# Performance work log

Hardware: AMD Instinct MI355X
Metric: run time of the kernel (lower is better)

The kernel has to match this reference:

```python
import jax, jax.numpy as jnp
import numpy as np

V = 50000  # word vocab (table has V+1 rows)
L = 256    # number of labels
B = 128    # batch
T = 512    # sequence length


def setup_inputs() -> dict:
    key = jax.random.key(0)
    k1, k2, k3 = jax.random.split(key, 3)
    emis = jax.random.normal(k1, (V + 1, L), dtype=jnp.float32)
    trans = jax.random.normal(k2, (L, L), dtype=jnp.float32)
    words = jax.random.randint(k3, (B, T), 0, V, dtype=jnp.int32)
    return {"emis": emis, "trans": trans, "words": words}


def reference(emis, trans, words):
    # Gather all emission scores up front: [B, T, L]
    e = emis[words]
    alpha0 = e[:, 0]  # [B, L]

    def step(alpha_prev, e_t):
        # alpha_new[b, c] = logsumexp_p( e_t[b, c] + trans[c, p] + alpha_prev[b, p] )
        scores = e_t[:, :, None] + trans[None, :, :] + alpha_prev[:, None, :]  # [B, L, L]
        return jax.nn.logsumexp(scores, axis=2), None

    # scan over time: e[:, 1:] -> time-major [T-1, B, L]
    alpha_last, _ = jax.lax.scan(step, alpha0, jnp.swapaxes(e[:, 1:], 0, 1))
    log_Z = jax.nn.logsumexp(alpha_last, axis=1).sum()  # scalar, summed over batch
    return log_Z
```

## Files before the change

### kernel.cpp

```cpp
#include <hip/hip_runtime.h>

#define NB 128
#define NT 512
#define NL 256
#define NWG NB

typedef float f32x4 __attribute__((ext_vector_type(4)));
typedef int   i32x8 __attribute__((ext_vector_type(8)));
typedef int   i32x4v __attribute__((ext_vector_type(4)));

#define EASTRIDE 272
#define GEXP 7
#define E8M0_ONE 127
#define INV_LN2 1.4426950408889634f
#define LN2 0.6931471805599453f

__device__ inline float log2_fast(float x) {
#if __has_builtin(__builtin_amdgcn_logf)
    return __builtin_amdgcn_logf(x);
#else
    return __log2f(x);
#endif
}
__device__ inline float exp2_fast(float x) {
#if __has_builtin(__builtin_amdgcn_exp2f)
    return __builtin_amdgcn_exp2f(x);
#else
    return exp2f(x);
#endif
}

__device__ inline void barrier_lds_only() {
    asm volatile("s_waitcnt lgkmcnt(0)" ::: "memory");
    __builtin_amdgcn_s_barrier();
    asm volatile("" ::: "memory");
}

__device__ inline unsigned pk_fp8x4(float a, float b, float c, float d) {
    int w = __builtin_amdgcn_cvt_pk_fp8_f32(a, b, 0, false);
    w     = __builtin_amdgcn_cvt_pk_fp8_f32(c, d, w, true);
    return (unsigned)w;
}

__device__ inline i32x8 ld_b256(const unsigned char* p) {
    i32x4v lo = *reinterpret_cast<const i32x4v*>(p);
    i32x4v hi = *reinterpret_cast<const i32x4v*>(p + 16);
    i32x8 r;
    r[0] = lo[0]; r[1] = lo[1]; r[2] = lo[2]; r[3] = lo[3];
    r[4] = hi[0]; r[5] = hi[1]; r[6] = hi[2]; r[7] = hi[3];
    return r;
}

__global__ __launch_bounds__(512, 2) void crf_forward(
    const float* __restrict__ emis,
    const float* __restrict__ trans,
    const int*   __restrict__ words,
    float*       __restrict__ bout)
{
    const int tid = threadIdx.x;
    const int l   = tid & 63;
    const int wv  = tid >> 6;
    const int g   = l >> 4;
    const int b   = l & 15;

    __shared__ __align__(16) unsigned char ea[2][EASTRIDE];
    __shared__ __align__(16) float pm[2][8];
    __shared__ int wlds[NT];

    const int wrow = blockIdx.x * NT;

    wlds[tid] = words[wrow + tid];

    i32x8 afr[2][2];
    #pragma unroll
    for (int T = 0; T < 2; ++T) {
        const int row = wv * 32 + T * 16 + b;
        #pragma unroll
        for (int kt = 0; kt < 2; ++kt) {
            const float* src = trans + row * NL + kt * 128 + g * 32;
            i32x8 a;
            #pragma unroll
            for (int w = 0; w < 8; ++w) {
                float4 v = *reinterpret_cast<const float4*>(src + w * 4);
                a[w] = (int)pk_fp8x4(__expf(v.x), __expf(v.y),
                                     __expf(v.z), __expf(v.w));
            }
            afr[T][kt] = a;
        }
    }

    const int w0 = words[wrow + 0];
    const int w1 = words[wrow + 1];
    const int w2 = words[wrow + 2];
    const int w3 = words[wrow + 3];
    const int w4 = words[wrow + 4];
    int wregA = words[wrow + 5];
    int wregB = words[wrow + 6];
    int wregC = words[wrow + 7];
    int wregD = words[wrow + 8];

    float S = 0.f;

    {
        const float* e0 = emis + (size_t)w0 * NL + wv * 32 + g * 4;
        float pmax = 0.f;
        unsigned pk[2];
        #pragma unroll
        for (int T = 0; T < 2; ++T) {
            f32x4 v = *reinterpret_cast<const f32x4*>(e0 + T * 16);
            float p0 = exp2_fast(v[0] * INV_LN2);
            float p1 = exp2_fast(v[1] * INV_LN2);
            float p2 = exp2_fast(v[2] * INV_LN2);
            float p3 = exp2_fast(v[3] * INV_LN2);
            pmax = fmaxf(pmax, fmaxf(fmaxf(p0, p1), fmaxf(p2, p3)));
            pk[T] = pk_fp8x4(p0, p1, p2, p3);
        }
        pmax = fmaxf(pmax, __shfl_xor(pmax, 16));
        pmax = fmaxf(pmax, __shfl_xor(pmax, 32));
        if (l == 0) pm[0][wv] = pmax;
        if (b == 0) {
            *reinterpret_cast<unsigned*>(&ea[0][wv * 32 + g * 4])      = pk[0];
            *reinterpret_cast<unsigned*>(&ea[0][wv * 32 + 16 + g * 4]) = pk[1];
        }
    }
    f32x4 pfA[2], pfB[2], pfC[2], pfD[2];
    {
        const float* p;
        p = emis + (size_t)w1 * NL + wv * 32 + g * 4;
        pfA[0] = *(const f32x4*)p; pfA[1] = *(const f32x4*)(p + 16);
        p = emis + (size_t)w2 * NL + wv * 32 + g * 4;
        pfB[0] = *(const f32x4*)p; pfB[1] = *(const f32x4*)(p + 16);
        p = emis + (size_t)w3 * NL + wv * 32 + g * 4;
        pfC[0] = *(const f32x4*)p; pfC[1] = *(const f32x4*)(p + 16);
        p = emis + (size_t)w4 * NL + wv * 32 + g * 4;
        pfD[0] = *(const f32x4*)p; pfD[1] = *(const f32x4*)(p + 16);
    }
    barrier_lds_only();

#define CRF_STEP(t, RD, WR, PF, WREG)                                           \
    {                                                                           \
                         \
        i32x8 bq0 = ld_b256(&ea[RD][g * 32]);                                   \
        i32x8 bq1 = ld_b256(&ea[RD][128 + g * 32]);                             \
        f32x4 pm0 = *reinterpret_cast<const f32x4*>(&pm[RD][0]);                \
        f32x4 pm1 = *reinterpret_cast<const f32x4*>(&pm[RD][4]);                \
        float gm  = fmaxf(fmaxf(fmaxf(pm0[0], pm0[1]), fmaxf(pm0[2], pm0[3])),  \
                          fmaxf(fmaxf(pm1[0], pm1[1]), fmaxf(pm1[2], pm1[3]))); \
        int   kb  = (int)(__builtin_bit_cast(unsigned, gm) >> 23) - (127 - GEXP);\
        S += (float)kb;                                                         \
        float kbf = (float)kb;                                                  \
        f32x4 eC[2] = { PF[0], PF[1] };                                         \
        if ((t) + 4 < NT) {                                                     \
            const float* ep = emis + (size_t)WREG * NL + wv * 32 + g * 4;       \
            PF[0] = *(const f32x4*)ep;  PF[1] = *(const f32x4*)(ep + 16);       \
        }                                                                       \
        if ((t) + 8 < NT) WREG = wlds[(t) + 8];                                 \
                                             \
        f32x4 ex[2];                                                            \
        _Pragma("unroll")                                                       \
        for (int T = 0; T < 2; ++T) {                                           \
            ex[T][0] = exp2_fast(fmaf(eC[T][0], INV_LN2, -kbf));                \
            ex[T][1] = exp2_fast(fmaf(eC[T][1], INV_LN2, -kbf));                \
            ex[T][2] = exp2_fast(fmaf(eC[T][2], INV_LN2, -kbf));                \
            ex[T][3] = exp2_fast(fmaf(eC[T][3], INV_LN2, -kbf));                \
        }                                                                       \
                      \
        f32x4 sA[2];                                                            \
        _Pragma("unroll")                                                       \
        for (int T = 0; T < 2; ++T) {                                           \
            f32x4 z = {0.f, 0.f, 0.f, 0.f};                                     \
            z = __builtin_amdgcn_mfma_scale_f32_16x16x128_f8f6f4(               \
                    afr[T][0], bq0, z, 0, 0, 0, E8M0_ONE, 0, E8M0_ONE);         \
            z = __builtin_amdgcn_mfma_scale_f32_16x16x128_f8f6f4(               \
                    afr[T][1], bq1, z, 0, 0, 0, E8M0_ONE, 0, E8M0_ONE);         \
            sA[T] = z;                                                          \
        }                                                                       \
        float pmax = 0.f;                                                       \
        unsigned pk[2];                                                         \
        _Pragma("unroll")                                                       \
        for (int T = 0; T < 2; ++T) {                                           \
            f32x4 wv4 = sA[T] * ex[T];                                          \
            pmax = fmaxf(pmax, fmaxf(fmaxf(wv4[0], wv4[1]),                     \
                                     fmaxf(wv4[2], wv4[3])));                   \
            pk[T] = pk_fp8x4(wv4[0], wv4[1], wv4[2], wv4[3]);                   \
        }                                                                       \
        pmax = fmaxf(pmax, __shfl_xor(pmax, 16));                               \
        pmax = fmaxf(pmax, __shfl_xor(pmax, 32));                               \
        if (l == 0) pm[WR][wv] = pmax;                                          \
        if (b == 0) {                                                           \
            *reinterpret_cast<unsigned*>(&ea[WR][wv * 32 + g * 4])      = pk[0];\
            *reinterpret_cast<unsigned*>(&ea[WR][wv * 32 + 16 + g * 4]) = pk[1];\
        }                                                                       \
        barrier_lds_only();                                                     \
    }

    int t = 1;
    for (; t + 3 < NT; t += 4) {
        CRF_STEP(t,     0, 1, pfA, wregA);
        CRF_STEP(t + 1, 1, 0, pfB, wregB);
        CRF_STEP(t + 2, 0, 1, pfC, wregC);
        CRF_STEP(t + 3, 1, 0, pfD, wregD);
    }
    CRF_STEP(509, 0, 1, pfA, wregA);
    CRF_STEP(510, 1, 0, pfB, wregB);
    CRF_STEP(511, 0, 1, pfC, wregC);
#undef CRF_STEP

    if (tid < 64) {
        unsigned u = *reinterpret_cast<const unsigned*>(&ea[1][tid * 4]);
        float s = __builtin_amdgcn_cvt_f32_fp8((int)u, 0)
                + __builtin_amdgcn_cvt_f32_fp8((int)u, 1)
                + __builtin_amdgcn_cvt_f32_fp8((int)u, 2)
                + __builtin_amdgcn_cvt_f32_fp8((int)u, 3);
        #pragma unroll
        for (int off = 32; off; off >>= 1) s += __shfl_xor(s, off);
        if (tid == 0) bout[blockIdx.x] = (S + log2_fast(s)) * LN2;
    }
}

__global__ void crf_reduce(const float* __restrict__ bout, float* __restrict__ out)
{
    const int tid = threadIdx.x;
    float v = bout[tid];
    #pragma unroll
    for (int off = 32; off; off >>= 1) v += __shfl_xor(v, off);
    __shared__ float sred[2];
    if ((tid & 63) == 0) sred[tid >> 6] = v;
    __syncthreads();
    if (tid == 0) out[0] = sred[0] + sred[1];
}

extern "C" void kernel_launch(void* const* d_in, const int* in_sizes, int n_in,
                              void* d_out, int out_size, void* d_ws, size_t ws_size,
                              hipStream_t stream)
{
    const float* emis  = (const float*)d_in[0];
    const float* trans = (const float*)d_in[1];
    const int*   words = (const int*)d_in[2];
    float* out  = (float*)d_out;
    float* bout = (float*)d_ws;

    crf_forward<<<NWG, 512, 0, stream>>>(emis, trans, words, bout);
    crf_reduce<<<1, NB, 0, stream>>>(bout, out);
}
```

Baseline: 293.2 us.

## Shorten emission prefetch depth, drop LDS word staging, interleave MFMA chains

Cuts the emission prefetch pipeline from four steps ahead to two, and reads word indices straight from global memory instead of staging them in LDS. The two independent MFMA accumulation chains are interleaved, the exp2 computations are moved ahead of the prefetch load, and the B-operand LDS loads become single 256-bit vector loads. The aim is to lower register pressure and LDS traffic on the serial recurrence's critical path. The risk is that the shallower prefetch exposes more global-load latency on each time step.

```diff
diff --git a/kernel.cpp b/kernel.cpp
--- a/kernel.cpp
+++ b/kernel.cpp
@@ -7,7 +7,6 @@
 
 typedef float f32x4 __attribute__((ext_vector_type(4)));
 typedef int   i32x8 __attribute__((ext_vector_type(8)));
-typedef int   i32x4v __attribute__((ext_vector_type(4)));
 
 #define EASTRIDE 272
 #define GEXP 7
@@ -40,15 +39,6 @@
     int w = __builtin_amdgcn_cvt_pk_fp8_f32(a, b, 0, false);
     w     = __builtin_amdgcn_cvt_pk_fp8_f32(c, d, w, true);
     return (unsigned)w;
-}
-
-__device__ inline i32x8 ld_b256(const unsigned char* p) {
-    i32x4v lo = *reinterpret_cast<const i32x4v*>(p);
-    i32x4v hi = *reinterpret_cast<const i32x4v*>(p + 16);
-    i32x8 r;
-    r[0] = lo[0]; r[1] = lo[1]; r[2] = lo[2]; r[3] = lo[3];
-    r[4] = hi[0]; r[5] = hi[1]; r[6] = hi[2]; r[7] = hi[3];
-    return r;
 }
 
 __global__ __launch_bounds__(512, 2) void crf_forward(
@@ -65,11 +55,9 @@
 
     __shared__ __align__(16) unsigned char ea[2][EASTRIDE];
     __shared__ __align__(16) float pm[2][8];
-    __shared__ int wlds[NT];
-
-    const int wrow = blockIdx.x * NT;
-
-    wlds[tid] = words[wrow + tid];
+
+    const int* ws = words + (size_t)blockIdx.x * NT;
+    const int eoff = wv * 32 + g * 4;
 
     i32x8 afr[2][2];
     #pragma unroll
@@ -89,121 +77,106 @@
         }
     }
 
-    const int w0 = words[wrow + 0];
-    const int w1 = words[wrow + 1];
-    const int w2 = words[wrow + 2];
-    const int w3 = words[wrow + 3];
-    const int w4 = words[wrow + 4];
-    int wregA = words[wrow + 5];
-    int wregB = words[wrow + 6];
-    int wregC = words[wrow + 7];
-    int wregD = words[wrow + 8];
+    const int w0 = ws[0];
+    const int w1 = ws[1];
+    const int w2 = ws[2];
+    int wA = ws[3];
+    int wB = ws[4];
 
     float S = 0.f;
 
     {
-        const float* e0 = emis + (size_t)w0 * NL + wv * 32 + g * 4;
-        float pmax = 0.f;
-        unsigned pk[2];
-        #pragma unroll
-        for (int T = 0; T < 2; ++T) {
-            f32x4 v = *reinterpret_cast<const f32x4*>(e0 + T * 16);
-            float p0 = exp2_fast(v[0] * INV_LN2);
-            float p1 = exp2_fast(v[1] * INV_LN2);
-            float p2 = exp2_fast(v[2] * INV_LN2);
-            float p3 = exp2_fast(v[3] * INV_LN2);
-            pmax = fmaxf(pmax, fmaxf(fmaxf(p0, p1), fmaxf(p2, p3)));
-            pk[T] = pk_fp8x4(p0, p1, p2, p3);
-        }
+        const float* e0 = emis + (size_t)w0 * NL + eoff;
+        f32x4 v0 = *reinterpret_cast<const f32x4*>(e0);
+        f32x4 v1 = *reinterpret_cast<const f32x4*>(e0 + 16);
+        float p00 = exp2_fast(v0[0] * INV_LN2), p01 = exp2_fast(v0[1] * INV_LN2);
+        float p02 = exp2_fast(v0[2] * INV_LN2), p03 = exp2_fast(v0[3] * INV_LN2);
+        float p10 = exp2_fast(v1[0] * INV_LN2), p11 = exp2_fast(v1[1] * INV_LN2);
+        float p12 = exp2_fast(v1[2] * INV_LN2), p13 = exp2_fast(v1[3] * INV_LN2);
+        float pmax = fmaxf(fmaxf(fmaxf(p00, p01), fmaxf(p02, p03)),
+                           fmaxf(fmaxf(p10, p11), fmaxf(p12, p13)));
         pmax = fmaxf(pmax, __shfl_xor(pmax, 16));
         pmax = fmaxf(pmax, __shfl_xor(pmax, 32));
         if (l == 0) pm[0][wv] = pmax;
         if (b == 0) {
-            *reinterpret_cast<unsigned*>(&ea[0][wv * 32 + g * 4])      = pk[0];
-            *reinterpret_cast<unsigned*>(&ea[0][wv * 32 + 16 + g * 4]) = pk[1];
+            *reinterpret_cast<unsigned*>(&ea[0][wv * 32 + g * 4]) =
+                pk_fp8x4(p00, p01, p02, p03);
+            *reinterpret_cast<unsigned*>(&ea[0][wv * 32 + 16 + g * 4]) =
+                pk_fp8x4(p10, p11, p12, p13);
         }
     }
-    f32x4 pfA[2], pfB[2], pfC[2], pfD[2];
+    f32x4 pfA0, pfA1, pfB0, pfB1;
     {
-        const float* p;
-        p = emis + (size_t)w1 * NL + wv * 32 + g * 4;
-        pfA[0] = *(const f32x4*)p; pfA[1] = *(const f32x4*)(p + 16);
-        p = emis + (size_t)w2 * NL + wv * 32 + g * 4;
-        pfB[0] = *(const f32x4*)p; pfB[1] = *(const f32x4*)(p + 16);
-        p = emis + (size_t)w3 * NL + wv * 32 + g * 4;
-        pfC[0] = *(const f32x4*)p; pfC[1] = *(const f32x4*)(p + 16);
-        p = emis + (size_t)w4 * NL + wv * 32 + g * 4;
-        pfD[0] = *(const f32x4*)p; pfD[1] = *(const f32x4*)(p + 16);
+        const float* p1 = emis + (size_t)w1 * NL + eoff;
+        pfA0 = *reinterpret_cast<const f32x4*>(p1);
+        pfA1 = *reinterpret_cast<const f32x4*>(p1 + 16);
+        const float* p2 = emis + (size_t)w2 * NL + eoff;
+        pfB0 = *reinterpret_cast<const f32x4*>(p2);
+        pfB1 = *reinterpret_cast<const f32x4*>(p2 + 16);
     }
     barrier_lds_only();
 
-#define CRF_STEP(t, RD, WR, PF, WREG)                                           \
+#define CRF_STEP(t, RD, WR, PF0, PF1, WREG)                                     \
     {                                                                           \
                          \
-        i32x8 bq0 = ld_b256(&ea[RD][g * 32]);                                   \
-        i32x8 bq1 = ld_b256(&ea[RD][128 + g * 32]);                             \
+        i32x8 bq0 = *reinterpret_cast<const i32x8*>(&ea[RD][g * 32]);           \
+        i32x8 bq1 = *reinterpret_cast<const i32x8*>(&ea[RD][128 + g * 32]);     \
         f32x4 pm0 = *reinterpret_cast<const f32x4*>(&pm[RD][0]);                \
         f32x4 pm1 = *reinterpret_cast<const f32x4*>(&pm[RD][4]);                \
-        float gm  = fmaxf(fmaxf(fmaxf(pm0[0], pm0[1]), fmaxf(pm0[2], pm0[3])),  \
-                          fmaxf(fmaxf(pm1[0], pm1[1]), fmaxf(pm1[2], pm1[3]))); \
-        int   kb  = (int)(__builtin_bit_cast(unsigned, gm) >> 23) - (127 - GEXP);\
+        float gm = fmaxf(fmaxf(fmaxf(pm0[0], pm0[1]), fmaxf(pm0[2], pm0[3])),   \
+                         fmaxf(fmaxf(pm1[0], pm1[1]), fmaxf(pm1[2], pm1[3])));  \
+        int   kb = (int)(__builtin_bit_cast(unsigned, gm) >> 23) - (127 - GEXP);\
         S += (float)kb;                                                         \
         float kbf = (float)kb;                                                  \
-        f32x4 eC[2] = { PF[0], PF[1] };                                         \
-        if ((t) + 4 < NT) {                                                     \
-            const float* ep = emis + (size_t)WREG * NL + wv * 32 + g * 4;       \
-            PF[0] = *(const f32x4*)ep;  PF[1] = *(const f32x4*)(ep + 16);       \
+             \
+        float exa0 = exp2_fast(fmaf(PF0[0], INV_LN2, -kbf));                    \
+        float exa1 = exp2_fast(fmaf(PF0[1], INV_LN2, -kbf));                    \
+        float exa2 = exp2_fast(fmaf(PF0[2], INV_LN2, -kbf));                    \
+        float exa3 = exp2_fast(fmaf(PF0[3], INV_LN2, -kbf));                    \
+        float exb0 = exp2_fast(fmaf(PF1[0], INV_LN2, -kbf));                    \
+        float exb1 = exp2_fast(fmaf(PF1[1], INV_LN2, -kbf));                    \
+        float exb2 = exp2_fast(fmaf(PF1[2], INV_LN2, -kbf));                    \
+        float exb3 = exp2_fast(fmaf(PF1[3], INV_LN2, -kbf));                    \
+        if ((t) + 2 < NT) {                                                     \
+            const float* ep = emis + (size_t)WREG * NL + eoff;                  \
+            PF0 = *reinterpret_cast<const f32x4*>(ep);                          \
+            PF1 = *reinterpret_cast<const f32x4*>(ep + 16);                     \
         }                                                                       \
-        if ((t) + 8 < NT) WREG = wlds[(t) + 8];                                 \
-                                             \
-        f32x4 ex[2];                                                            \
-        _Pragma("unroll")                                                       \
-        for (int T = 0; T < 2; ++T) {                                           \
-            ex[T][0] = exp2_fast(fmaf(eC[T][0], INV_LN2, -kbf));                \
-            ex[T][1] = exp2_fast(fmaf(eC[T][1], INV_LN2, -kbf));                \
-            ex[T][2] = exp2_fast(fmaf(eC[T][2], INV_LN2, -kbf));                \
-            ex[T][3] = exp2_fast(fmaf(eC[T][3], INV_LN2, -kbf));                \
-        }                                                                       \
-                      \
-        f32x4 sA[2];                                                            \
-        _Pragma("unroll")                                                       \
-        for (int T = 0; T < 2; ++T) {                                           \
-            f32x4 z = {0.f, 0.f, 0.f, 0.f};                                     \
-            z = __builtin_amdgcn_mfma_scale_f32_16x16x128_f8f6f4(               \
-                    afr[T][0], bq0, z, 0, 0, 0, E8M0_ONE, 0, E8M0_ONE);         \
-            z = __builtin_amdgcn_mfma_scale_f32_16x16x128_f8f6f4(               \
-                    afr[T][1], bq1, z, 0, 0, 0, E8M0_ONE, 0, E8M0_ONE);         \
-            sA[T] = z;                                                          \
-        }                                                                       \
-        float pmax = 0.f;                                                       \
-        unsigned pk[2];                                                         \
-        _Pragma("unroll")                                                       \
-        for (int T = 0; T < 2; ++T) {                                           \
-            f32x4 wv4 = sA[T] * ex[T];                                          \
-            pmax = fmaxf(pmax, fmaxf(fmaxf(wv4[0], wv4[1]),                     \
-                                     fmaxf(wv4[2], wv4[3])));                   \
-            pk[T] = pk_fp8x4(wv4[0], wv4[1], wv4[2], wv4[3]);                   \
-        }                                                                       \
+        if ((t) + 4 < NT) WREG = ws[(t) + 4];                                   \
+                         \
+        f32x4 z0 = {0.f, 0.f, 0.f, 0.f};                                        \
+        f32x4 z1 = {0.f, 0.f, 0.f, 0.f};                                        \
+        z0 = __builtin_amdgcn_mfma_scale_f32_16x16x128_f8f6f4(                  \
+                 afr[0][0], bq0, z0, 0, 0, 0, E8M0_ONE, 0, E8M0_ONE);           \
+        z1 = __builtin_amdgcn_mfma_scale_f32_16x16x128_f8f6f4(                  \
+                 afr[1][0], bq0, z1, 0, 0, 0, E8M0_ONE, 0, E8M0_ONE);           \
+        z0 = __builtin_amdgcn_mfma_scale_f32_16x16x128_f8f6f4(                  \
+                 afr[0][1], bq1, z0, 0, 0, 0, E8M0_ONE, 0, E8M0_ONE);           \
+        z1 = __builtin_amdgcn_mfma_scale_f32_16x16x128_f8f6f4(                  \
+                 afr[1][1], bq1, z1, 0, 0, 0, E8M0_ONE, 0, E8M0_ONE);           \
+        float v00 = z0[0] * exa0, v01 = z0[1] * exa1;                           \
+        float v02 = z0[2] * exa2, v03 = z0[3] * exa3;                           \
+        float v10 = z1[0] * exb0, v11 = z1[1] * exb1;                           \
+        float v12 = z1[2] * exb2, v13 = z1[3] * exb3;                           \
+        float pmax = fmaxf(fmaxf(fmaxf(v00, v01), fmaxf(v02, v03)),             \
+                           fmaxf(fmaxf(v10, v11), fmaxf(v12, v13)));            \
         pmax = fmaxf(pmax, __shfl_xor(pmax, 16));                               \
         pmax = fmaxf(pmax, __shfl_xor(pmax, 32));                               \
         if (l == 0) pm[WR][wv] = pmax;                                          \
         if (b == 0) {                                                           \
-            *reinterpret_cast<unsigned*>(&ea[WR][wv * 32 + g * 4])      = pk[0];\
-            *reinterpret_cast<unsigned*>(&ea[WR][wv * 32 + 16 + g * 4]) = pk[1];\
+            *reinterpret_cast<unsigned*>(&ea[WR][wv * 32 + g * 4]) =            \
+                pk_fp8x4(v00, v01, v02, v03);                                   \
+            *reinterpret_cast<unsigned*>(&ea[WR][wv * 32 + 16 + g * 4]) =       \
+                pk_fp8x4(v10, v11, v12, v13);                                   \
         }                                                                       \
         barrier_lds_only();                                                     \
     }
 
-    int t = 1;
-    for (; t + 3 < NT; t += 4) {
-        CRF_STEP(t,     0, 1, pfA, wregA);
-        CRF_STEP(t + 1, 1, 0, pfB, wregB);
-        CRF_STEP(t + 2, 0, 1, pfC, wregC);
-        CRF_STEP(t + 3, 1, 0, pfD, wregD);
-    }
-    CRF_STEP(509, 0, 1, pfA, wregA);
-    CRF_STEP(510, 1, 0, pfB, wregB);
-    CRF_STEP(511, 0, 1, pfC, wregC);
+    for (int t = 1; t + 1 < NT; t += 2) {
+        CRF_STEP(t,     0, 1, pfA0, pfA1, wA);
+        CRF_STEP(t + 1, 1, 0, pfB0, pfB1, wB);
+    }
+    CRF_STEP(511, 0, 1, pfA0, pfA1, wA);
 #undef CRF_STEP
 
     if (tid < 64) {
```

New measurement: 308.2 us. 5.1% more time.
